# Kernel tuning notes

Hardware: AMD Instinct MI355X
Metric: run time of the kernel (lower is better)

The kernel has to match this reference:

```python
import jax, jax.numpy as jnp
import numpy as np

B, S, D = 32, 128, 1024      # encoder batch, seq len, embed_dim
C = 65536                    # nclasses (sense inventory)
N = 512                      # number of gathered WSD target tokens
NNZ = 262144                 # nnz of sparse label adjacency A (avg degree 4)
EPS = 1e-5                   # BatchNorm1d eps


def setup_inputs() -> dict:
    key = jax.random.key(0)
    ks = jax.random.split(key, 7)
    enc_out = jax.random.normal(ks[0], (B, S, D), dtype=jnp.float32)
    batch_idx = jax.random.randint(ks[1], (N,), 0, B)
    tgt = jax.random.randint(ks[2], (N,), 0, S)
    A_indices = jax.random.randint(ks[3], (2, NNZ), 0, C)
    A_values = jax.random.uniform(ks[4], (NNZ,), dtype=jnp.float32)
    wt2_w = jax.random.normal(ks[5], (C, D), dtype=jnp.float32) / np.sqrt(D).astype(np.float32)
    wt2_b = jax.random.normal(ks[6], (C,), dtype=jnp.float32) * 0.02
    return {"enc_out": enc_out, "wt2_w": wt2_w, "wt2_b": wt2_b,
            "A_values": A_values, "batch_idx": batch_idx, "tgt": tgt,
            "A_indices": A_indices}


def reference(enc_out, wt2_w, wt2_b, A_values, batch_idx, tgt, A_indices):
    # gather target-token embeddings: [N, D]
    g = enc_out[batch_idx, tgt]
    # BatchNorm1d(affine=False), training mode -> batch stats, biased var
    mean = jnp.mean(g, axis=0)
    var = jnp.var(g, axis=0)
    h0 = (g - mean) / jnp.sqrt(var + EPS)
    # wt2 Linear + swish -> logits over classes Z: [N, C]
    h1 = jax.nn.swish(h0 @ wt2_w.T + wt2_b)
    # sparse spmm: torch_sparse.spmm(ii, vv, m=C, n=C, matrix=Z.T).T == Z @ A.T
    row, col = A_indices[0], A_indices[1]
    gathered = h1.T[col] * A_values[:, None]            # [NNZ, N]
    neighbors = jax.ops.segment_sum(gathered, row, num_segments=C).T  # [N, C]
    # residual add (renormalize=False)
    return neighbors + h1
```

## Files before the change

### kernel.cpp

```cpp
#include <hip/hip_runtime.h>
#include <hip/hip_bf16.h>

typedef unsigned short u16;
typedef unsigned int   u32;
typedef __attribute__((ext_vector_type(8))) short bf16x8;
typedef __attribute__((ext_vector_type(4))) float f32x4;

static constexpr int kS = 128, kD = 1024, kC = 65536, kN = 512, kNNZ = 262144;

__device__ __forceinline__ u16 f2bf(float x) {
  u32 u = __float_as_uint(x);
  u32 r = (u + 0x7fffu + ((u >> 16) & 1u)) >> 16;
  return (u16)r;
}
__device__ __forceinline__ u32 pack2(float a, float b) {
  return (u32)f2bf(a) | ((u32)f2bf(b) << 16);
}
__device__ __forceinline__ u32 pk(float a, float b) {
  __hip_bfloat162 h = __float22bfloat162_rn(float2{a, b});
  union { __hip_bfloat162 v; u32 u; } c; c.v = h;
  return c.u;
}
__device__ __forceinline__ float bf_lo(u32 v) { return __uint_as_float(v << 16); }
__device__ __forceinline__ float bf_hi(u32 v) { return __uint_as_float(v & 0xffff0000u); }

__global__ void k_bn_part(const float* __restrict__ enc, const int* __restrict__ bidx,
                          const int* __restrict__ tgt, float* __restrict__ part) {
  __shared__ int offs[64];
  int n0 = blockIdx.y * 64;
  if (threadIdx.x < 64) offs[threadIdx.x] = bidx[n0 + threadIdx.x] * kS + tgt[n0 + threadIdx.x];
  __syncthreads();
  int d = blockIdx.x * 256 + threadIdx.x;
  float s = 0.f, ss = 0.f;
  for (int i = 0; i < 64; ++i) {
    float v = enc[(size_t)offs[i] * kD + d];
    s += v; ss += v * v;
  }
  part[(blockIdx.y * 2 + 0) * kD + d] = s;
  part[(blockIdx.y * 2 + 1) * kD + d] = ss;
}

__global__ void k_bn_fin(const float* __restrict__ part, float* __restrict__ mean,
                         float* __restrict__ rstd) {
  int d = blockIdx.x * 256 + threadIdx.x;
  float s = 0.f, ss = 0.f;
#pragma unroll
  for (int b = 0; b < 8; ++b) {
    s  += part[(b * 2 + 0) * kD + d];
    ss += part[(b * 2 + 1) * kD + d];
  }
  float m = s * (1.f / kN);
  float var = ss * (1.f / kN) - m * m;
  mean[d] = m;
  rstd[d] = 1.f / sqrtf(var + 1e-5f);
}

__global__ void k_bn_pack(const float* __restrict__ enc, const int* __restrict__ bidx,
                          const int* __restrict__ tgt, const float* __restrict__ mean,
                          const float* __restrict__ rstd, u16* __restrict__ Bp) {
  int i = blockIdx.x * 256 + threadIdx.x;
  int n = i & 511;
  int g = i >> 9;
  int k0 = g * 8;
  size_t src = (size_t)(bidx[n] * kS + tgt[n]) * kD + k0;
  float4 v0 = *(const float4*)(enc + src);
  float4 v1 = *(const float4*)(enc + src + 4);
  float4 m0 = *(const float4*)(mean + k0);
  float4 m1 = *(const float4*)(mean + k0 + 4);
  float4 r0 = *(const float4*)(rstd + k0);
  float4 r1 = *(const float4*)(rstd + k0 + 4);
  u32 q0 = pack2((v0.x - m0.x) * r0.x, (v0.y - m0.y) * r0.y);
  u32 q1 = pack2((v0.z - m0.z) * r0.z, (v0.w - m0.w) * r0.w);
  u32 q2 = pack2((v1.x - m1.x) * r1.x, (v1.y - m1.y) * r1.y);
  u32 q3 = pack2((v1.z - m1.z) * r1.z, (v1.w - m1.w) * r1.w);
  *(uint4*)(Bp + (size_t)i * 8) = make_uint4(q0, q1, q2, q3);
}

__global__ void k_hist(const int* __restrict__ rows, int* __restrict__ hist) {
  int e = blockIdx.x * blockDim.x + threadIdx.x;
  if (e < kNNZ) atomicAdd(&hist[rows[e]], 1);
}

__global__ __launch_bounds__(1024) void k_scan(int* __restrict__ hist, int* __restrict__ cursor) {
  __shared__ int sm[1024];
  int t = threadIdx.x;
  int base = t * 64;
  int sum = 0;
  for (int i = 0; i < 64; ++i) sum += hist[base + i];
  sm[t] = sum;
  __syncthreads();
  for (int off = 1; off < 1024; off <<= 1) {
    int v = (t >= off) ? sm[t - off] : 0;
    __syncthreads();
    sm[t] += v;
    __syncthreads();
  }
  int run = sm[t] - sum;
  for (int i = 0; i < 64; ++i) {
    int v = hist[base + i];
    hist[base + i] = run;
    cursor[base + i] = run;
    run += v;
  }
  if (t == 1023) hist[kC] = run;
}

__global__ void k_scatter(const int* __restrict__ rows, const int* __restrict__ cols,
                          const float* __restrict__ vals, int* __restrict__ cursor,
                          int* __restrict__ scol, float* __restrict__ sval) {
  int e = blockIdx.x * blockDim.x + threadIdx.x;
  if (e < kNNZ) {
    int r = rows[e];
    int p = atomicAdd(&cursor[r], 1);
    scol[p] = cols[e];
    sval[p] = vals[e];
  }
}

__global__ __launch_bounds__(512, 4)
void k_gemm_f5(const float* __restrict__ W, const u16* __restrict__ Bp,
               const float* __restrict__ bias, u16* __restrict__ h1t) {
  __shared__ __align__(16) u16 Ab[2 * 64 * 64];
  const int t = threadIdx.x;
  const int l = t & 63, w = t >> 6;
  const int wn = w * 64;
  const int cb = blockIdx.x * 64;
  const int q = l >> 4, ln = l & 15;

  const int sr = t >> 3, sc = t & 7;
  const float* gA = W + (size_t)(cb + sr) * kD + sc * 8;
  const int swoff = sr * 64 + ((sc ^ (sr & 7)) * 8);

  const u16* gB = Bp + (size_t)q * 4096 + (size_t)(wn + ln) * 8;

  f32x4 acc[4][4];
#pragma unroll
  for (int a = 0; a < 4; ++a)
#pragma unroll
    for (int b = 0; b < 4; ++b) acc[a][b] = (f32x4){0.f, 0.f, 0.f, 0.f};

  {
    float4 a0 = *(const float4*)(gA);
    float4 a1 = *(const float4*)(gA + 4);
    *(uint4*)(Ab + swoff) =
        make_uint4(pk(a0.x, a0.y), pk(a0.z, a0.w), pk(a1.x, a1.y), pk(a1.z, a1.w));
  }
  __syncthreads();

#pragma unroll 2
  for (int tt = 0; tt < 16; ++tt) {
    const int cur = tt & 1;
    float4 na0, na1;
    if (tt < 15) {
      na0 = *(const float4*)(gA + (tt + 1) * 64);
      na1 = *(const float4*)(gA + (tt + 1) * 64 + 4);
    }
    const u16* curb = Ab + cur * 4096;
#pragma unroll
    for (int ks = 0; ks < 2; ++ks) {
      bf16x8 bv[4];
#pragma unroll
      for (int nb = 0; nb < 4; ++nb)
        bv[nb] = *(const bf16x8*)(gB + (size_t)((tt * 8 + ks * 4) * 4096) + nb * 128);
#pragma unroll
      for (int mb = 0; mb < 4; ++mb) {
        int rr = mb * 16 + ln;
        bf16x8 af = *(const bf16x8*)(curb + rr * 64 + (((ks * 4 + q) ^ (rr & 7)) * 8));
#pragma unroll
        for (int nb = 0; nb < 4; ++nb)
          acc[mb][nb] = __builtin_amdgcn_mfma_f32_16x16x32_bf16(af, bv[nb], acc[mb][nb], 0, 0, 0);
      }
    }
    if (tt < 15) {
      *(uint4*)(Ab + (cur ^ 1) * 4096 + swoff) =
          make_uint4(pk(na0.x, na0.y), pk(na0.z, na0.w), pk(na1.x, na1.y), pk(na1.z, na1.w));
    }
    __syncthreads();
  }

#pragma unroll
  for (int mb = 0; mb < 4; ++mb) {
    int rb = mb * 16 + q * 4;
#pragma unroll
    for (int i = 0; i < 4; ++i) {
      int c = cb + rb + i;
      float bvs = bias[c];
#pragma unroll
      for (int nb = 0; nb < 4; ++nb) {
        float x = acc[mb][nb][i] + bvs;
        float sw = x / (1.f + __expf(-x));
        h1t[(size_t)c * kN + (wn + nb * 16 + ln)] = f2bf(sw);
      }
    }
  }
}

#define FMA8(cv, v)                                                        \
  a0 = fmaf(v, bf_lo(cv.x), a0); a1 = fmaf(v, bf_hi(cv.x), a1);            \
  a2 = fmaf(v, bf_lo(cv.y), a2); a3 = fmaf(v, bf_hi(cv.y), a3);            \
  a4 = fmaf(v, bf_lo(cv.z), a4); a5 = fmaf(v, bf_hi(cv.z), a5);            \
  a6 = fmaf(v, bf_lo(cv.w), a6); a7 = fmaf(v, bf_hi(cv.w), a7);

__global__ __launch_bounds__(512)
void k_spmm(const u16* __restrict__ h1t, const int* __restrict__ rowptr,
            const int* __restrict__ scol, const float* __restrict__ sval,
            float* __restrict__ out) {
  __shared__ float tile[32 * 512];
  int r0 = blockIdx.x * 32;
  int t = threadIdx.x, w = t >> 6, l = t & 63;
#pragma unroll
  for (int j = 0; j < 4; ++j) {
    int rl = w * 4 + j;
    int r = r0 + rl;
    uint4 hv = ((const uint4*)(h1t + (size_t)r * kN))[l];
    float a0 = bf_lo(hv.x), a1 = bf_hi(hv.x), a2 = bf_lo(hv.y), a3 = bf_hi(hv.y);
    float a4 = bf_lo(hv.z), a5 = bf_hi(hv.z), a6 = bf_lo(hv.w), a7 = bf_hi(hv.w);
    int e0 = rowptr[r], e1 = rowptr[r + 1];
    uint4 cv0 = {}, cv1 = {};
    float v0 = 0.f, v1 = 0.f;
    if (e0 < e1) {
      v0 = sval[e0];
      cv0 = ((const uint4*)(h1t + (size_t)scol[e0] * kN))[l];
    }
    if (e0 + 1 < e1) {
      v1 = sval[e0 + 1];
      cv1 = ((const uint4*)(h1t + (size_t)scol[e0 + 1] * kN))[l];
    }
    for (int e = e0; e < e1; e += 2) {
      FMA8(cv0, v0);
      if (e + 2 < e1) {
        v0 = sval[e + 2];
        cv0 = ((const uint4*)(h1t + (size_t)scol[e + 2] * kN))[l];
      }
      if (e + 1 < e1) {
        FMA8(cv1, v1);
        if (e + 3 < e1) {
          v1 = sval[e + 3];
          cv1 = ((const uint4*)(h1t + (size_t)scol[e + 3] * kN))[l];
        }
      }
    }
    int sw = (rl & 7) << 2;
    *(float4*)&tile[rl * 512 + ((8 * l) ^ sw)]     = make_float4(a0, a1, a2, a3);
    *(float4*)&tile[rl * 512 + ((8 * l + 4) ^ sw)] = make_float4(a4, a5, a6, a7);
  }
  __syncthreads();
  int r = l & 31;
  int swr = (r & 7) << 2;
#pragma unroll
  for (int it = 0; it < 32; ++it) {
    int n = it * 16 + w * 2 + (l >> 5);
    out[(size_t)n * kC + r0 + r] = tile[r * 512 + (n ^ swr)];
  }
}

extern "C" void kernel_launch(void* const* d_in, const int* in_sizes, int n_in,
                              void* d_out, int out_size, void* d_ws, size_t ws_size,
                              hipStream_t stream) {
  (void)in_sizes; (void)n_in; (void)out_size; (void)ws_size;
  const float* enc   = (const float*)d_in[0];
  const float* W     = (const float*)d_in[1];
  const float* bias  = (const float*)d_in[2];
  const float* Avals = (const float*)d_in[3];
  const int*   bidx  = (const int*)d_in[4];
  const int*   tgt   = (const int*)d_in[5];
  const int*   Arow  = (const int*)d_in[6];
  const int*   Acol  = Arow + kNNZ;
  float* out = (float*)d_out;

  char* ws = (char*)d_ws;
  float* mean   = (float*)(ws);
  float* rstd   = (float*)(ws + 4096);
  u16*   Bp     = (u16*)  (ws + 8192);
  int*   rowptr = (int*)  (ws + 1056768);
  int*   cursor = (int*)  (ws + 1319168);
  int*   scol   = (int*)  (ws + 1581312);
  float* sval   = (float*)(ws + 2629888);
  float* part   = (float*)(ws + 3678464);
  u16*   h1t    = (u16*)  (ws + 4194304);

  hipMemsetAsync(rowptr, 0, (kC + 1) * sizeof(int), stream);
  k_bn_part<<<dim3(4, 8), 256, 0, stream>>>(enc, bidx, tgt, part);
  k_bn_fin<<<4, 256, 0, stream>>>(part, mean, rstd);
  k_bn_pack<<<256, 256, 0, stream>>>(enc, bidx, tgt, mean, rstd, Bp);
  k_hist<<<kNNZ / 256, 256, 0, stream>>>(Arow, rowptr);
  k_scan<<<1, 1024, 0, stream>>>(rowptr, cursor);
  k_scatter<<<kNNZ / 256, 256, 0, stream>>>(Arow, Acol, Avals, cursor, scol, sval);
  k_gemm_f5<<<kC / 64, 512, 0, stream>>>(W, Bp, bias, h1t);
  k_spmm<<<kC / 32, 512, 0, stream>>>(h1t, rowptr, scol, sval, out);
}
```

Measured before the change: 294.4 us.

## Stage fp32 weight tiles via global_load_lds and split GEMM N across blocks

The weight GEMM now copies fp32 W tiles straight into LDS with global_load_lds (async direct-to-LDS, XOR-swizzled) and converts them to bf16 when fragments are read, rather than loading into registers, converting, then storing to LDS. The grid splits the 512 N columns across two 256-thread blocks per 64-row class tile, so each block holds half the B operand range. The aim is to cut register staging and VGPR pressure and to improve overlap of loads with MFMA. In exchange, LDS footprint doubles (fp32 tiles), bf16 conversion is repeated in the inner loop, and each W tile is now read from global memory by two blocks.

```diff
diff --git a/kernel.cpp b/kernel.cpp
--- a/kernel.cpp
+++ b/kernel.cpp
@@ -23,6 +23,12 @@
 }
 __device__ __forceinline__ float bf_lo(u32 v) { return __uint_as_float(v << 16); }
 __device__ __forceinline__ float bf_hi(u32 v) { return __uint_as_float(v & 0xffff0000u); }
+
+__device__ __forceinline__ void gload16(const void* g, void* l) {
+  __builtin_amdgcn_global_load_lds(
+      (const __attribute__((address_space(1))) void*)g,
+      (__attribute__((address_space(3))) void*)l, 16, 0, 0);
+}
 
 __global__ void k_bn_part(const float* __restrict__ enc, const int* __restrict__ bidx,
                           const int* __restrict__ tgt, float* __restrict__ part) {
@@ -117,21 +123,27 @@
   }
 }
 
-__global__ __launch_bounds__(512, 4)
-void k_gemm_f5(const float* __restrict__ W, const u16* __restrict__ Bp,
+__global__ __launch_bounds__(256, 4)
+void k_gemm_f6(const float* __restrict__ W, const u16* __restrict__ Bp,
                const float* __restrict__ bias, u16* __restrict__ h1t) {
-  __shared__ __align__(16) u16 Ab[2 * 64 * 64];
+  __shared__ __align__(16) float Ab[2][64 * 64];
   const int t = threadIdx.x;
   const int l = t & 63, w = t >> 6;
   const int wn = w * 64;
-  const int cb = blockIdx.x * 64;
+  const int cb = blockIdx.y * 64;
+  const int nb0 = blockIdx.x * 256;
   const int q = l >> 4, ln = l & 15;
 
-  const int sr = t >> 3, sc = t & 7;
-  const float* gA = W + (size_t)(cb + sr) * kD + sc * 8;
-  const int swoff = sr * 64 + ((sc ^ (sr & 7)) * 8);
-
-  const u16* gB = Bp + (size_t)q * 4096 + (size_t)(wn + ln) * 8;
+  const float* gs0; const float* gs1; const float* gs2; const float* gs3;
+  {
+    int s0 = t, s1 = t + 256, s2 = t + 512, s3 = t + 768;
+    gs0 = W + (size_t)(cb + (s0 >> 4)) * kD + ((s0 & 15) ^ ((s0 >> 4) & 15)) * 4;
+    gs1 = W + (size_t)(cb + (s1 >> 4)) * kD + ((s1 & 15) ^ ((s1 >> 4) & 15)) * 4;
+    gs2 = W + (size_t)(cb + (s2 >> 4)) * kD + ((s2 & 15) ^ ((s2 >> 4) & 15)) * 4;
+    gs3 = W + (size_t)(cb + (s3 >> 4)) * kD + ((s3 & 15) ^ ((s3 >> 4) & 15)) * 4;
+  }
+
+  const u16* gB = Bp + ((size_t)q * 512 + nb0 + wn + ln) * 8;
 
   f32x4 acc[4][4];
 #pragma unroll
@@ -139,41 +151,44 @@
 #pragma unroll
     for (int b = 0; b < 4; ++b) acc[a][b] = (f32x4){0.f, 0.f, 0.f, 0.f};
 
-  {
-    float4 a0 = *(const float4*)(gA);
-    float4 a1 = *(const float4*)(gA + 4);
-    *(uint4*)(Ab + swoff) =
-        make_uint4(pk(a0.x, a0.y), pk(a0.z, a0.w), pk(a1.x, a1.y), pk(a1.z, a1.w));
-  }
+  gload16(gs0, (char*)Ab[0] + (t + 0) * 16);
+  gload16(gs1, (char*)Ab[0] + (t + 256) * 16);
+  gload16(gs2, (char*)Ab[0] + (t + 512) * 16);
+  gload16(gs3, (char*)Ab[0] + (t + 768) * 16);
   __syncthreads();
 
 #pragma unroll 2
   for (int tt = 0; tt < 16; ++tt) {
     const int cur = tt & 1;
-    float4 na0, na1;
     if (tt < 15) {
-      na0 = *(const float4*)(gA + (tt + 1) * 64);
-      na1 = *(const float4*)(gA + (tt + 1) * 64 + 4);
-    }
-    const u16* curb = Ab + cur * 4096;
+      int go = (tt + 1) * 64;
+      char* nb_ = (char*)Ab[cur ^ 1];
+      gload16(gs0 + go, nb_ + (t + 0) * 16);
+      gload16(gs1 + go, nb_ + (t + 256) * 16);
+      gload16(gs2 + go, nb_ + (t + 512) * 16);
+      gload16(gs3 + go, nb_ + (t + 768) * 16);
+    }
+    const float* curb = Ab[cur];
 #pragma unroll
     for (int ks = 0; ks < 2; ++ks) {
       bf16x8 bv[4];
 #pragma unroll
       for (int nb = 0; nb < 4; ++nb)
-        bv[nb] = *(const bf16x8*)(gB + (size_t)((tt * 8 + ks * 4) * 4096) + nb * 128);
+        bv[nb] = *(const bf16x8*)(gB + (size_t)(tt * 8 + ks * 4) * 4096 + nb * 128);
 #pragma unroll
       for (int mb = 0; mb < 4; ++mb) {
         int rr = mb * 16 + ln;
-        bf16x8 af = *(const bf16x8*)(curb + rr * 64 + (((ks * 4 + q) ^ (rr & 7)) * 8));
+        int sb = ks * 8 + q * 2;
+        const float4* rowp = (const float4*)(curb + rr * 64);
+        float4 a0 = rowp[(sb + 0) ^ (rr & 15)];
+        float4 a1 = rowp[(sb + 1) ^ (rr & 15)];
+        union { u32 u[4]; bf16x8 v; } cv;
+        cv.u[0] = pk(a0.x, a0.y); cv.u[1] = pk(a0.z, a0.w);
+        cv.u[2] = pk(a1.x, a1.y); cv.u[3] = pk(a1.z, a1.w);
 #pragma unroll
         for (int nb = 0; nb < 4; ++nb)
-          acc[mb][nb] = __builtin_amdgcn_mfma_f32_16x16x32_bf16(af, bv[nb], acc[mb][nb], 0, 0, 0);
+          acc[mb][nb] = __builtin_amdgcn_mfma_f32_16x16x32_bf16(cv.v, bv[nb], acc[mb][nb], 0, 0, 0);
       }
-    }
-    if (tt < 15) {
-      *(uint4*)(Ab + (cur ^ 1) * 4096 + swoff) =
-          make_uint4(pk(na0.x, na0.y), pk(na0.z, na0.w), pk(na1.x, na1.y), pk(na1.z, na1.w));
     }
     __syncthreads();
   }
@@ -189,7 +204,7 @@
       for (int nb = 0; nb < 4; ++nb) {
         float x = acc[mb][nb][i] + bvs;
         float sw = x / (1.f + __expf(-x));
-        h1t[(size_t)c * kN + (wn + nb * 16 + ln)] = f2bf(sw);
+        h1t[(size_t)c * kN + (nb0 + wn + nb * 16 + ln)] = f2bf(sw);
       }
     }
   }
@@ -286,6 +301,6 @@
   k_hist<<<kNNZ / 256, 256, 0, stream>>>(Arow, rowptr);
   k_scan<<<1, 1024, 0, stream>>>(rowptr, cursor);
   k_scatter<<<kNNZ / 256, 256, 0, stream>>>(Arow, Acol, Avals, cursor, scol, sval);
-  k_gemm_f5<<<kC / 64, 512, 0, stream>>>(W, Bp, bias, h1t);
+  k_gemm_f6<<<dim3(2, 1024), 256, 0, stream>>>(W, Bp, bias, h1t);
   k_spmm<<<kC / 32, 512, 0, stream>>>(h1t, rowptr, scol, sval, out);
 }
```

After: 364.0 us. 1.24x slower.

## Stage B operand in LDS via global_load_lds and enlarge GEMM tile to 128 classes

Applied to the files above, without the earlier changes.

The wt2 GEMM kernel now uses 1024-thread blocks covering 128 classes, with two wave rows sharing each B tile. The packed activation matrix B is staged into double-buffered LDS through direct global-to-LDS loads instead of being read from global memory per wave. K steps shrink to 32 and run over 32 iterations. This cuts redundant global/L2 traffic for B and halves the block count. The cost is larger LDS use (about 80KB per block), lower occupancy, and more barriers.

```diff
diff --git a/kernel.cpp b/kernel.cpp
--- a/kernel.cpp
+++ b/kernel.cpp
@@ -23,6 +23,12 @@
 }
 __device__ __forceinline__ float bf_lo(u32 v) { return __uint_as_float(v << 16); }
 __device__ __forceinline__ float bf_hi(u32 v) { return __uint_as_float(v & 0xffff0000u); }
+
+__device__ __forceinline__ void gload16(const void* g, void* l) {
+  __builtin_amdgcn_global_load_lds(
+      (const __attribute__((address_space(1))) void*)g,
+      (__attribute__((address_space(3))) void*)l, 16, 0, 0);
+}
 
 __global__ void k_bn_part(const float* __restrict__ enc, const int* __restrict__ bidx,
                           const int* __restrict__ tgt, float* __restrict__ part) {
@@ -117,21 +123,23 @@
   }
 }
 
-__global__ __launch_bounds__(512, 4)
-void k_gemm_f5(const float* __restrict__ W, const u16* __restrict__ Bp,
+__global__ __launch_bounds__(1024, 4)
+void k_gemm_f7(const float* __restrict__ W, const u16* __restrict__ Bp,
                const float* __restrict__ bias, u16* __restrict__ h1t) {
-  __shared__ __align__(16) u16 Ab[2 * 64 * 64];
+  __shared__ __align__(16) u16 Bb[2][16384];
+  __shared__ __align__(16) u16 Ab[2][4096];
   const int t = threadIdx.x;
   const int l = t & 63, w = t >> 6;
-  const int wn = w * 64;
-  const int cb = blockIdx.x * 64;
+  const int wm = w >> 3, wn = (w & 7) * 64;
+  const int cb = blockIdx.x * 128;
   const int q = l >> 4, ln = l & 15;
 
-  const int sr = t >> 3, sc = t & 7;
-  const float* gA = W + (size_t)(cb + sr) * kD + sc * 8;
-  const int swoff = sr * 64 + ((sc ^ (sr & 7)) * 8);
-
-  const u16* gB = Bp + (size_t)q * 4096 + (size_t)(wn + ln) * 8;
+  const u16* gB0 = Bp + (size_t)t * 8;
+  const u16* gB1 = Bp + (size_t)(t + 1024) * 8;
+
+  const int sr = t >> 2;
+  const float* gA = W + (size_t)(cb + sr) * kD + (t & 3) * 8;
+  const int aws = sr * 32 + (((t & 3) ^ (sr & 3)) * 8);
 
   f32x4 acc[4][4];
 #pragma unroll
@@ -139,40 +147,44 @@
 #pragma unroll
     for (int b = 0; b < 4; ++b) acc[a][b] = (f32x4){0.f, 0.f, 0.f, 0.f};
 
-  {
+  gload16(gB0, (char*)Bb[0] + t * 16);
+  gload16(gB1, (char*)Bb[0] + (t + 1024) * 16);
+  if (t < 512) {
     float4 a0 = *(const float4*)(gA);
     float4 a1 = *(const float4*)(gA + 4);
-    *(uint4*)(Ab + swoff) =
+    *(uint4*)(&Ab[0][aws]) =
         make_uint4(pk(a0.x, a0.y), pk(a0.z, a0.w), pk(a1.x, a1.y), pk(a1.z, a1.w));
   }
   __syncthreads();
 
 #pragma unroll 2
-  for (int tt = 0; tt < 16; ++tt) {
+  for (int tt = 0; tt < 32; ++tt) {
     const int cur = tt & 1;
     float4 na0, na1;
-    if (tt < 15) {
-      na0 = *(const float4*)(gA + (tt + 1) * 64);
-      na1 = *(const float4*)(gA + (tt + 1) * 64 + 4);
-    }
-    const u16* curb = Ab + cur * 4096;
-#pragma unroll
-    for (int ks = 0; ks < 2; ++ks) {
-      bf16x8 bv[4];
+    if (tt < 31) {
+      gload16(gB0 + (size_t)(tt + 1) * 16384, (char*)Bb[cur ^ 1] + t * 16);
+      gload16(gB1 + (size_t)(tt + 1) * 16384, (char*)Bb[cur ^ 1] + (t + 1024) * 16);
+      if (t < 512) {
+        na0 = *(const float4*)(gA + (tt + 1) * 32);
+        na1 = *(const float4*)(gA + (tt + 1) * 32 + 4);
+      }
+    }
+    bf16x8 bv[4], af[4];
+#pragma unroll
+    for (int nb = 0; nb < 4; ++nb)
+      bv[nb] = *(const bf16x8*)(&Bb[cur][(q * 512 + wn + nb * 16 + ln) * 8]);
+#pragma unroll
+    for (int mb = 0; mb < 4; ++mb) {
+      int rr = wm * 64 + mb * 16 + ln;
+      af[mb] = *(const bf16x8*)(&Ab[cur][rr * 32 + ((q ^ (rr & 3)) * 8)]);
+    }
+#pragma unroll
+    for (int mb = 0; mb < 4; ++mb)
 #pragma unroll
       for (int nb = 0; nb < 4; ++nb)
-        bv[nb] = *(const bf16x8*)(gB + (size_t)((tt * 8 + ks * 4) * 4096) + nb * 128);
-#pragma unroll
-      for (int mb = 0; mb < 4; ++mb) {
-        int rr = mb * 16 + ln;
-        bf16x8 af = *(const bf16x8*)(curb + rr * 64 + (((ks * 4 + q) ^ (rr & 7)) * 8));
-#pragma unroll
-        for (int nb = 0; nb < 4; ++nb)
-          acc[mb][nb] = __builtin_amdgcn_mfma_f32_16x16x32_bf16(af, bv[nb], acc[mb][nb], 0, 0, 0);
-      }
-    }
-    if (tt < 15) {
-      *(uint4*)(Ab + (cur ^ 1) * 4096 + swoff) =
+        acc[mb][nb] = __builtin_amdgcn_mfma_f32_16x16x32_bf16(af[mb], bv[nb], acc[mb][nb], 0, 0, 0);
+    if (tt < 31 && t < 512) {
+      *(uint4*)(&Ab[cur ^ 1][aws]) =
           make_uint4(pk(na0.x, na0.y), pk(na0.z, na0.w), pk(na1.x, na1.y), pk(na1.z, na1.w));
     }
     __syncthreads();
@@ -180,7 +192,7 @@
 
 #pragma unroll
   for (int mb = 0; mb < 4; ++mb) {
-    int rb = mb * 16 + q * 4;
+    int rb = wm * 64 + mb * 16 + q * 4;
 #pragma unroll
     for (int i = 0; i < 4; ++i) {
       int c = cb + rb + i;
@@ -286,6 +298,6 @@
   k_hist<<<kNNZ / 256, 256, 0, stream>>>(Arow, rowptr);
   k_scan<<<1, 1024, 0, stream>>>(rowptr, cursor);
   k_scatter<<<kNNZ / 256, 256, 0, stream>>>(Arow, Acol, Avals, cursor, scol, sval);
-  k_gemm_f5<<<kC / 64, 512, 0, stream>>>(W, Bp, bias, h1t);
+  k_gemm_f7<<<512, 1024, 0, stream>>>(W, Bp, bias, h1t);
   k_spmm<<<kC / 32, 512, 0, stream>>>(h1t, rowptr, scol, sval, out);
 }
```

New measurement: 293.1 us. About the same (-0.4%).
